# Optimization experiments

Hardware: AMD Instinct MI355X
Metric: run time of the kernel (lower is better)

Reference implementation:

```python
import jax, jax.numpy as jnp
import numpy as np

B, S, D = 2, 4096, 1024
P_DROP = 0.2


def setup_inputs() -> dict:
    key = jax.random.key(0)
    ks = jax.random.split(key, 8)
    scale = 1.0 / np.sqrt(D)
    return {
        "x": jax.random.normal(ks[0], (B, S, D), jnp.float32),
        "Wq": jax.random.normal(ks[1], (D, D), jnp.float32) * scale,
        "bq": jnp.zeros((D,), jnp.float32),
        "Wk": jax.random.normal(ks[2], (D, D), jnp.float32) * scale,
        "bk": jnp.zeros((D,), jnp.float32),
        "Wv": jax.random.normal(ks[3], (D, D), jnp.float32) * scale,
        "bv": jnp.zeros((D,), jnp.float32),
        "dropout_u": jax.random.uniform(ks[4], (B, S, S), jnp.float32),
    }


def reference(x, Wq, bq, Wk, bk, Wv, bv, dropout_u):
    # torch nn.Linear: y = x @ W.T + b
    Q = jnp.einsum("bsd,ed->bse", x, Wq) + bq
    K = jnp.einsum("bsd,ed->bse", x, Wk) + bk
    V = jnp.einsum("bsd,ed->bse", x, Wv) + bv
    # NOTE: original has no 1/sqrt(d) scaling
    scores = jnp.einsum("bqd,bkd->bqk", Q, K)  # [B,S,S]
    attn = jax.nn.softmax(scores, axis=-1)
    # inverted dropout, p=0.2, deterministic mask from dropout_u
    mask = (dropout_u >= P_DROP).astype(attn.dtype) / (1.0 - P_DROP)
    attn = attn * mask
    return jnp.einsum("bqk,bkd->bqd", attn, V)
```

## Files before the change

kernel.cpp:

```cpp
#include <hip/hip_runtime.h>

typedef float    f32x4 __attribute__((ext_vector_type(4)));
typedef _Float16 f16x8 __attribute__((ext_vector_type(8)));
typedef _Float16 f16x4 __attribute__((ext_vector_type(4)));
typedef _Float16 f16;

#define DEVFN static __device__ __forceinline__

constexpr int BB = 2, SS = 4096, DD = 1024;
constexpr int MROWS = BB * SS;

constexpr size_t SZ_QK   = (size_t)MROWS * DD * 2;
constexpr size_t SZ_VT   = (size_t)BB * DD * SS * 2;
constexpr size_t SZ_ATTN = (size_t)BB * SS * SS * 2;
constexpr size_t SZ_S    = (size_t)BB * SS * SS * 4;
constexpr size_t SZ_W    = (size_t)DD * DD * 2;

constexpr size_t O_VT   = 0;
constexpr size_t O_ATTN = O_VT + SZ_VT;
constexpr size_t O_Q    = O_ATTN;
constexpr size_t O_K    = O_Q + 2 * SZ_QK;
constexpr size_t O_S    = O_ATTN + SZ_ATTN;
constexpr size_t O_XH   = O_S;
constexpr size_t O_WQH  = O_XH + SZ_QK;
constexpr size_t O_WKH  = O_WQH + SZ_W;
constexpr size_t O_WVH  = O_WKH + SZ_W;
constexpr size_t WS_NEEDED = SZ_VT + SZ_ATTN + SZ_S;

DEVFN f32x4 mfma16x16x32(f16x8 a, f16x8 b, f32x4 c) {
  return __builtin_amdgcn_mfma_f32_16x16x32_f16(a, b, c, 0, 0, 0);
}

DEVFN void gld16(const f16* g, char* l) {
  __builtin_amdgcn_global_load_lds((const __attribute__((address_space(1))) void*)g,
                                   (__attribute__((address_space(3))) void*)l, 16, 0, 0);
}

DEVFN void swz_xy(int& bx, int& by, int& bz) {
  const int gx = gridDim.x, gy = gridDim.y, gz = gridDim.z;
  const int lin = (blockIdx.z * gy + blockIdx.y) * gx + blockIdx.x;
  const int chunk = (gx * gy * gz) >> 3;
  const int nl = (lin & 7) * chunk + (lin >> 3);
  bx = nl % gx; const int r = nl / gx; by = r % gy; bz = r / gy;
}

DEVFN void gemm128_core(const f16* Ap, const f16* Bp, size_t ld, int NT,
                        char* smem, f32x4 (&acc)[4][4]) {
  const int tid = threadIdx.x, lane = tid & 63, wave = tid >> 6;
  const int wm = wave >> 1, wn = wave & 1;
  const size_t rk = (size_t)(tid >> 3) * ld +
                    (size_t)((((lane & 7) ^ (lane >> 3)) << 3));
  const int wvoff = wave << 10;
  const int rbA = (((wm << 6) + (lane & 15)) << 7);
  const int rbB = (((wn << 6) + (lane & 15)) << 7);
  const int cx0 = (((lane >> 4) << 4)) ^ ((lane & 7) << 4);
  const int cx1 = cx0 ^ 64;

  char* LA0 = smem;
  char* LA1 = smem + 32768;
  char* LA2 = smem + 65536;
  char* LB0 = smem + 98304;
  char* LB1 = smem + 114688;

  auto stA = [&](int u, int q, char* dst) {
    int uc = (u < NT) ? u : (NT - 1);
    gld16(Ap + (size_t)(q << 6) * ld + ((size_t)uc << 6) + rk, dst + (q << 13) + wvoff);
  };
  auto stB = [&](int u, int q, char* dst) {
    int uc = (u < NT) ? u : (NT - 1);
    gld16(Bp + (size_t)(q << 6) * ld + ((size_t)uc << 6) + rk, dst + (q << 13) + wvoff);
  };
  auto rdA = [&](char* l, int m, int cx) { return *(const f16x8*)(l + rbA + (m << 11) + cx); };
  auto rdB = [&](char* l, int n, int cx) { return *(const f16x8*)(l + rbB + (n << 11) + cx); };

  f16x8 A0[2][2], B0[2][2], A0n[2][2], B0n[2][2];

  stA(0, 0, LA0); stA(0, 1, LA0); stA(0, 2, LA0); stA(0, 3, LA0);
  stB(0, 0, LB0); stB(0, 1, LB0);
  stA(1, 0, LA1); stA(1, 1, LA1); stA(1, 2, LA1); stA(1, 3, LA1);
  stB(1, 0, LB1); stB(1, 1, LB1);
  asm volatile("s_waitcnt vmcnt(6)" ::: "memory");
  __builtin_amdgcn_s_barrier();
#pragma unroll
  for (int n = 0; n < 2; ++n) { B0[n][0] = rdB(LB0, n, cx0); B0[n][1] = rdB(LB0, n, cx1); }
#pragma unroll
  for (int m = 0; m < 2; ++m) { A0[m][0] = rdA(LA0, m, cx0); A0[m][1] = rdA(LA0, m, cx1); }

  char *aC = LA0, *aN = LA1, *aN2 = LA2, *bC = LB0, *bN = LB1;

  auto tileX = [&](char* lA, char* lB, char* lAn, char* lA2, char* lBn, int t,
                   f16x8 (&a0)[2][2], f16x8 (&b0)[2][2],
                   f16x8 (&a0n)[2][2], f16x8 (&b0n)[2][2]) {
    f16x8 a1[2][2], b1[2][2];
#pragma unroll
    for (int n = 0; n < 2; ++n) { b1[n][0] = rdB(lB, n + 2, cx0); b1[n][1] = rdB(lB, n + 2, cx1); }
    stA(t + 2, 0, lA2); stA(t + 2, 1, lA2);
    __builtin_amdgcn_s_barrier();
    asm volatile("s_waitcnt lgkmcnt(4)" ::: "memory");
    __builtin_amdgcn_sched_barrier(0);
    __builtin_amdgcn_s_setprio(1);
#pragma unroll
    for (int m = 0; m < 2; ++m)
#pragma unroll
      for (int n = 0; n < 2; ++n) {
        acc[m][n] = mfma16x16x32(a0[m][0], b0[n][0], acc[m][n]);
        acc[m][n] = mfma16x16x32(a0[m][1], b0[n][1], acc[m][n]);
      }
    __builtin_amdgcn_s_setprio(0);
    __builtin_amdgcn_s_barrier();
#pragma unroll
    for (int m = 0; m < 2; ++m) { a1[m][0] = rdA(lA, m + 2, cx0); a1[m][1] = rdA(lA, m + 2, cx1); }
    stA(t + 2, 2, lA2); stA(t + 2, 3, lA2);
    asm volatile("s_waitcnt vmcnt(4)" ::: "memory");
    __builtin_amdgcn_s_barrier();
    asm volatile("s_waitcnt lgkmcnt(4)" ::: "memory");
    __builtin_amdgcn_sched_barrier(0);
    __builtin_amdgcn_s_setprio(1);
#pragma unroll
    for (int m = 0; m < 2; ++m)
#pragma unroll
      for (int n = 0; n < 2; ++n) {
        acc[m][n + 2] = mfma16x16x32(a0[m][0], b1[n][0], acc[m][n + 2]);
        acc[m][n + 2] = mfma16x16x32(a0[m][1], b1[n][1], acc[m][n + 2]);
      }
    __builtin_amdgcn_s_setprio(0);
    __builtin_amdgcn_s_barrier();
#pragma unroll
    for (int n = 0; n < 2; ++n) { b0n[n][0] = rdB(lBn, n, cx0); b0n[n][1] = rdB(lBn, n, cx1); }
    stB(t + 2, 0, lB); stB(t + 2, 1, lB);
    __builtin_amdgcn_s_barrier();
    asm volatile("s_waitcnt lgkmcnt(4)" ::: "memory");
    __builtin_amdgcn_sched_barrier(0);
    __builtin_amdgcn_s_setprio(1);
#pragma unroll
    for (int m = 0; m < 2; ++m)
#pragma unroll
      for (int n = 0; n < 2; ++n) {
        acc[m + 2][n] = mfma16x16x32(a1[m][0], b0[n][0], acc[m + 2][n]);
        acc[m + 2][n] = mfma16x16x32(a1[m][1], b0[n][1], acc[m + 2][n]);
      }
    __builtin_amdgcn_s_setprio(0);
    __builtin_amdgcn_s_barrier();
#pragma unroll
    for (int m = 0; m < 2; ++m) { a0n[m][0] = rdA(lAn, m, cx0); a0n[m][1] = rdA(lAn, m, cx1); }
    __builtin_amdgcn_s_barrier();
    asm volatile("s_waitcnt lgkmcnt(4)" ::: "memory");
    __builtin_amdgcn_sched_barrier(0);
    __builtin_amdgcn_s_setprio(1);
#pragma unroll
    for (int m = 0; m < 2; ++m)
#pragma unroll
      for (int n = 0; n < 2; ++n) {
        acc[m + 2][n + 2] = mfma16x16x32(a1[m][0], b1[n][0], acc[m + 2][n + 2]);
        acc[m + 2][n + 2] = mfma16x16x32(a1[m][1], b1[n][1], acc[m + 2][n + 2]);
      }
    __builtin_amdgcn_s_setprio(0);
    __builtin_amdgcn_s_barrier();
  };

  for (int t = 0; t < NT; t += 2) {
    tileX(aC, bC, aN, aN2, bN, t, A0, B0, A0n, B0n);
    { char* tmp = aC; aC = aN; aN = aN2; aN2 = tmp; }
    { char* tmp = bC; bC = bN; bN = tmp; }
    tileX(aC, bC, aN, aN2, bN, t + 1, A0n, B0n, A0, B0);
    { char* tmp = aC; aC = aN; aN = aN2; aN2 = tmp; }
    { char* tmp = bC; bC = bN; bN = tmp; }
  }
  asm volatile("s_waitcnt vmcnt(0)" ::: "memory");
}

__global__ __launch_bounds__(512, 2)
void gemm_sc128(const f16* __restrict__ Q, const f16* __restrict__ Kp,
                float* __restrict__ Sf) {
  extern __shared__ char smem[];
  int bx, by, bz; swz_xy(bx, by, bz);
  const size_t zo = (size_t)bz * SS * DD;
  const int row0 = by * 256, col0 = bx * 128;
  f32x4 acc[4][4] = {};
  gemm128_core(Q + zo + (size_t)row0 * DD, Kp + zo + (size_t)col0 * DD,
               DD, 16, smem, acc);

  float* C = Sf + (size_t)bz * SS * SS;
  const int lane = threadIdx.x & 63, wave = threadIdx.x >> 6;
  const int wm = wave >> 1, wn = wave & 1;
#pragma unroll
  for (int m = 0; m < 4; ++m)
#pragma unroll
    for (int n = 0; n < 4; ++n) {
      int col = col0 + wn * 64 + n * 16 + (lane & 15);
      int rowb = row0 + wm * 64 + m * 16 + (lane >> 4) * 4;
#pragma unroll
      for (int j = 0; j < 4; ++j)
        __builtin_nontemporal_store(acc[m][n][j], &C[(size_t)(rowb + j) * SS + col]);
    }
}

__global__ __launch_bounds__(512, 2)
void gemm_projqk128(const f16* __restrict__ xh,
                    const f16* __restrict__ wqh, const f16* __restrict__ wkh,
                    const float* __restrict__ bq, const float* __restrict__ bk,
                    f16* __restrict__ Q, f16* __restrict__ K) {
  extern __shared__ char smem[];
  int bx, by, bz; swz_xy(bx, by, bz);
  const int row0 = by * 256;
  const bool isK = bx >= 8;
  const int col0 = (bx & 7) * 128;
  const f16* B0p = isK ? wkh : wqh;
  const float* bias = isK ? bk : bq;
  f16* CH = isK ? K : Q;

  f32x4 acc[4][4] = {};
  gemm128_core(xh + (size_t)row0 * DD, B0p + (size_t)col0 * DD, DD, 16, smem, acc);

  const int lane = threadIdx.x & 63, wave = threadIdx.x >> 6;
  const int wm = wave >> 1, wn = wave & 1;
#pragma unroll
  for (int m = 0; m < 4; ++m)
#pragma unroll
    for (int n = 0; n < 4; ++n) {
      int col = col0 + wn * 64 + n * 16 + (lane & 15);
      float bvv = bias[col];
      int rowb = row0 + wm * 64 + m * 16 + (lane >> 4) * 4;
#pragma unroll
      for (int j = 0; j < 4; ++j)
        CH[(size_t)(rowb + j) * DD + col] = (f16)(acc[m][n][j] + bvv);
    }
}

__global__ __launch_bounds__(512, 2)
void gemm_vt128(const f16* __restrict__ wvh, const f16* __restrict__ xh,
                const float* __restrict__ bvv, f16* __restrict__ Vt) {
  extern __shared__ char smem[];
  int bx, by, bz; swz_xy(bx, by, bz);
  const int row0 = by * 256;
  const int col0 = bx * 128;
  f32x4 acc[4][4] = {};
  gemm128_core(wvh + (size_t)row0 * DD, xh + (size_t)col0 * DD, DD, 16, smem, acc);

  const int lane = threadIdx.x & 63, wave = threadIdx.x >> 6;
  const int wm = wave >> 1, wn = wave & 1;
#pragma unroll
  for (int m = 0; m < 4; ++m)
#pragma unroll
    for (int n = 0; n < 4; ++n) {
      int col = col0 + wn * 64 + n * 16 + (lane & 15);
      int batch = col >> 12, sl = col & 4095;
      int rowb = row0 + wm * 64 + m * 16 + (lane >> 4) * 4;
#pragma unroll
      for (int j = 0; j < 4; ++j) {
        float v = acc[m][n][j] + bvv[rowb + j];
        Vt[(size_t)batch * DD * SS + (size_t)(rowb + j) * SS + sl] = (f16)v;
      }
    }
}

__global__ __launch_bounds__(512, 2)
void gemm_pv128(const f16* __restrict__ Pb, const f16* __restrict__ Vt,
                float* __restrict__ out) {
  extern __shared__ char smem[];
  int bx, by, bz; swz_xy(bx, by, bz);
  const int row0 = by * 256;
  const int col0 = bx * 128;
  f32x4 acc[4][4] = {};
  gemm128_core(Pb + (size_t)bz * SS * SS + (size_t)row0 * SS,
               Vt + (size_t)bz * DD * SS + (size_t)col0 * SS,
               SS, 64, smem, acc);

  float* C = out + (size_t)bz * SS * DD;
  const int lane = threadIdx.x & 63, wave = threadIdx.x >> 6;
  const int wm = wave >> 1, wn = wave & 1;
#pragma unroll
  for (int m = 0; m < 4; ++m)
#pragma unroll
    for (int n = 0; n < 4; ++n) {
      int col = col0 + wn * 64 + n * 16 + (lane & 15);
      int rowb = row0 + wm * 64 + m * 16 + (lane >> 4) * 4;
#pragma unroll
      for (int j = 0; j < 4; ++j)
        __builtin_nontemporal_store(acc[m][n][j], &C[(size_t)(rowb + j) * DD + col]);
    }
}

__global__ __launch_bounds__(256)
void split_all(const float* __restrict__ x, const float* __restrict__ Wq,
               const float* __restrict__ Wk, const float* __restrict__ Wv,
               f16* __restrict__ xh, f16* __restrict__ wqh,
               f16* __restrict__ wkh, f16* __restrict__ wvh) {
  const int b = blockIdx.x, tid = threadIdx.x;
  const float* in; f16* hi; int nv, rb, nb;
  if (b < 1536)      { in = x;  hi = xh;  nv = (MROWS * DD) >> 2; rb = b;        nb = 1536; }
  else if (b < 1792) { in = Wq; hi = wqh; nv = (DD * DD) >> 2;    rb = b - 1536; nb = 256; }
  else if (b < 2048) { in = Wk; hi = wkh; nv = (DD * DD) >> 2;    rb = b - 1792; nb = 256; }
  else               { in = Wv; hi = wvh; nv = (DD * DD) >> 2;    rb = b - 2048; nb = 256; }
  for (int i = rb * 256 + tid; i < nv; i += nb * 256) {
    f32x4 v = *(const f32x4*)(in + (size_t)i * 4);
    f16x4 h;
#pragma unroll
    for (int e = 0; e < 4; ++e) h[e] = (f16)v[e];
    *(f16x4*)(hi + (size_t)i * 4) = h;
  }
}

__global__ __launch_bounds__(256)
void softmax_dropout(const float* __restrict__ Sf, const float* __restrict__ U,
                     f16* __restrict__ P) {
  __shared__ float red[4];
  const size_t row = blockIdx.x;
  const float* s = Sf + row * SS;
  const float* u = U + row * SS;
  f16* p = P + row * SS;
  const int tid = threadIdx.x, lane = tid & 63, wave = tid >> 6;

  f32x4 v[4];
  float m = -3.0e38f;
#pragma unroll
  for (int j = 0; j < 4; ++j) {
    v[j] = __builtin_nontemporal_load((const f32x4*)(s + (size_t)(j * 256 + tid) * 4));
#pragma unroll
    for (int e = 0; e < 4; ++e) m = fmaxf(m, v[j][e]);
  }
#pragma unroll
  for (int o = 32; o > 0; o >>= 1) m = fmaxf(m, __shfl_xor(m, o));
  if (lane == 0) red[wave] = m;
  __syncthreads();
  m = fmaxf(fmaxf(red[0], red[1]), fmaxf(red[2], red[3]));

  float sum = 0.0f;
#pragma unroll
  for (int j = 0; j < 4; ++j)
#pragma unroll
    for (int e = 0; e < 4; ++e) { float ex = __expf(v[j][e] - m); v[j][e] = ex; sum += ex; }
#pragma unroll
  for (int o = 32; o > 0; o >>= 1) sum += __shfl_xor(sum, o);
  __syncthreads();
  if (lane == 0) red[wave] = sum;
  __syncthreads();
  sum = red[0] + red[1] + red[2] + red[3];
  const float scale = 1.25f / sum;

#pragma unroll
  for (int j = 0; j < 4; ++j) {
    f32x4 uu = __builtin_nontemporal_load((const f32x4*)(u + (size_t)(j * 256 + tid) * 4));
    f16x4 out;
#pragma unroll
    for (int e = 0; e < 4; ++e)
      out[e] = (f16)((uu[e] >= 0.2f) ? v[j][e] * scale : 0.0f);
    *(f16x4*)(p + (size_t)(j * 256 + tid) * 4) = out;
  }
}

extern "C" void kernel_launch(void* const* d_in, const int* in_sizes, int n_in,
                              void* d_out, int out_size, void* d_ws, size_t ws_size,
                              hipStream_t stream) {
  if (ws_size < WS_NEEDED) return;

  const float* x  = (const float*)d_in[0];
  const float* Wq = (const float*)d_in[1];
  const float* bq = (const float*)d_in[2];
  const float* Wk = (const float*)d_in[3];
  const float* bk = (const float*)d_in[4];
  const float* Wv = (const float*)d_in[5];
  const float* bv = (const float*)d_in[6];
  const float* du = (const float*)d_in[7];

  char* ws = (char*)d_ws;
  f16*   Vt  = (f16*)(ws + O_VT);
  f16*   Pb  = (f16*)(ws + O_ATTN);
  f16*   Q   = (f16*)(ws + O_Q);
  f16*   K   = (f16*)(ws + O_K);
  float* Sf  = (float*)(ws + O_S);
  f16*   xh  = (f16*)(ws + O_XH);
  f16*   wqh = (f16*)(ws + O_WQH);
  f16*   wkh = (f16*)(ws + O_WKH);
  f16*   wvh = (f16*)(ws + O_WVH);
  float* out = (float*)d_out;

  hipFuncSetAttribute((const void*)gemm_sc128,
                      hipFuncAttributeMaxDynamicSharedMemorySize, 131072);
  hipFuncSetAttribute((const void*)gemm_projqk128,
                      hipFuncAttributeMaxDynamicSharedMemorySize, 131072);
  hipFuncSetAttribute((const void*)gemm_vt128,
                      hipFuncAttributeMaxDynamicSharedMemorySize, 131072);
  hipFuncSetAttribute((const void*)gemm_pv128,
                      hipFuncAttributeMaxDynamicSharedMemorySize, 131072);

  split_all<<<2304, 256, 0, stream>>>(x, Wq, Wk, Wv, xh, wqh, wkh, wvh);

  gemm_projqk128<<<dim3(16, MROWS / 256), 512, 131072, stream>>>(
      xh, wqh, wkh, bq, bk, Q, K);

  gemm_vt128<<<dim3(MROWS / 128, DD / 256), 512, 131072, stream>>>(wvh, xh, bv, Vt);

  gemm_sc128<<<dim3(SS / 128, SS / 256, BB), 512, 131072, stream>>>(Q, K, Sf);

  softmax_dropout<<<MROWS, 256, 0, stream>>>(Sf, du, Pb);

  gemm_pv128<<<dim3(DD / 128, SS / 256, BB), 512, 131072, stream>>>(Pb, Vt, out);
}
```

Baseline: 276.0 us.

## Merge QK and V projection GEMMs into one launch and remap score-GEMM blocks

Merges the Q/K projection kernel and the V-transpose projection kernel into a single 768-block launch, with block ids interleaved across groups of 8. It also replaces the score GEMM's block swizzle with a custom mapping that groups 128 tiles per XCD-style region, and drops the nontemporal stores for the fp32 score matrix. The aim is to cut one launch and tail, balance work across the chip, and keep score tiles cache-resident for the softmax that follows. Removing the nontemporal hint may push useful data out of cache.

```diff
diff --git a/kernel.cpp b/kernel.cpp
--- a/kernel.cpp
+++ b/kernel.cpp
@@ -173,7 +173,13 @@
 void gemm_sc128(const f16* __restrict__ Q, const f16* __restrict__ Kp,
                 float* __restrict__ Sf) {
   extern __shared__ char smem[];
-  int bx, by, bz; swz_xy(bx, by, bz);
+  const int lin = (blockIdx.z * 16 + blockIdx.y) * 32 + blockIdx.x;
+  const int g = (lin & 7) * 128 + (lin >> 3);
+  const int bz = g >> 9;
+  const int w = g & 511;
+  const int t = w >> 7, s = w & 127;
+  const int bx = (t & 1) * 16 + (s & 15);
+  const int by = (t >> 1) * 8 + (s >> 4);
   const size_t zo = (size_t)bz * SS * DD;
   const int row0 = by * 256, col0 = bx * 128;
   f32x4 acc[4][4] = {};
@@ -191,67 +197,64 @@
       int rowb = row0 + wm * 64 + m * 16 + (lane >> 4) * 4;
 #pragma unroll
       for (int j = 0; j < 4; ++j)
-        __builtin_nontemporal_store(acc[m][n][j], &C[(size_t)(rowb + j) * SS + col]);
+        C[(size_t)(rowb + j) * SS + col] = acc[m][n][j];
     }
 }
 
 __global__ __launch_bounds__(512, 2)
-void gemm_projqk128(const f16* __restrict__ xh,
+void gemm_projvt128(const f16* __restrict__ xh,
                     const f16* __restrict__ wqh, const f16* __restrict__ wkh,
+                    const f16* __restrict__ wvh,
                     const float* __restrict__ bq, const float* __restrict__ bk,
-                    f16* __restrict__ Q, f16* __restrict__ K) {
+                    const float* __restrict__ bvv,
+                    f16* __restrict__ Q, f16* __restrict__ K,
+                    f16* __restrict__ Vt) {
   extern __shared__ char smem[];
-  int bx, by, bz; swz_xy(bx, by, bz);
-  const int row0 = by * 256;
-  const bool isK = bx >= 8;
-  const int col0 = (bx & 7) * 128;
-  const f16* B0p = isK ? wkh : wqh;
-  const float* bias = isK ? bk : bq;
-  f16* CH = isK ? K : Q;
-
-  f32x4 acc[4][4] = {};
-  gemm128_core(xh + (size_t)row0 * DD, B0p + (size_t)col0 * DD, DD, 16, smem, acc);
-
+  const int lin = blockIdx.x;
+  const int id = (lin & 7) * 96 + (lin >> 3);
   const int lane = threadIdx.x & 63, wave = threadIdx.x >> 6;
   const int wm = wave >> 1, wn = wave & 1;
-#pragma unroll
-  for (int m = 0; m < 4; ++m)
-#pragma unroll
-    for (int n = 0; n < 4; ++n) {
-      int col = col0 + wn * 64 + n * 16 + (lane & 15);
-      float bvv = bias[col];
-      int rowb = row0 + wm * 64 + m * 16 + (lane >> 4) * 4;
-#pragma unroll
-      for (int j = 0; j < 4; ++j)
-        CH[(size_t)(rowb + j) * DD + col] = (f16)(acc[m][n][j] + bvv);
-    }
-}
-
-__global__ __launch_bounds__(512, 2)
-void gemm_vt128(const f16* __restrict__ wvh, const f16* __restrict__ xh,
-                const float* __restrict__ bvv, f16* __restrict__ Vt) {
-  extern __shared__ char smem[];
-  int bx, by, bz; swz_xy(bx, by, bz);
-  const int row0 = by * 256;
-  const int col0 = bx * 128;
   f32x4 acc[4][4] = {};
-  gemm128_core(wvh + (size_t)row0 * DD, xh + (size_t)col0 * DD, DD, 16, smem, acc);
-
-  const int lane = threadIdx.x & 63, wave = threadIdx.x >> 6;
-  const int wm = wave >> 1, wn = wave & 1;
-#pragma unroll
-  for (int m = 0; m < 4; ++m)
-#pragma unroll
-    for (int n = 0; n < 4; ++n) {
-      int col = col0 + wn * 64 + n * 16 + (lane & 15);
-      int batch = col >> 12, sl = col & 4095;
-      int rowb = row0 + wm * 64 + m * 16 + (lane >> 4) * 4;
-#pragma unroll
-      for (int j = 0; j < 4; ++j) {
-        float v = acc[m][n][j] + bvv[rowb + j];
-        Vt[(size_t)batch * DD * SS + (size_t)(rowb + j) * SS + sl] = (f16)v;
-      }
-    }
+
+  if (id < 512) {
+    const int bx = id & 15, by = id >> 4;
+    const int row0 = by * 256;
+    const bool isK = bx >= 8;
+    const int col0 = (bx & 7) * 128;
+    const f16* B0p = isK ? wkh : wqh;
+    const float* bias = isK ? bk : bq;
+    f16* CH = isK ? K : Q;
+    gemm128_core(xh + (size_t)row0 * DD, B0p + (size_t)col0 * DD, DD, 16, smem, acc);
+#pragma unroll
+    for (int m = 0; m < 4; ++m)
+#pragma unroll
+      for (int n = 0; n < 4; ++n) {
+        int col = col0 + wn * 64 + n * 16 + (lane & 15);
+        float bvv2 = bias[col];
+        int rowb = row0 + wm * 64 + m * 16 + (lane >> 4) * 4;
+#pragma unroll
+        for (int j = 0; j < 4; ++j)
+          CH[(size_t)(rowb + j) * DD + col] = (f16)(acc[m][n][j] + bvv2);
+      }
+  } else {
+    const int id2 = id - 512;
+    const int bx = id2 & 63, by = id2 >> 6;
+    const int row0 = by * 256, col0 = bx * 128;
+    gemm128_core(wvh + (size_t)row0 * DD, xh + (size_t)col0 * DD, DD, 16, smem, acc);
+#pragma unroll
+    for (int m = 0; m < 4; ++m)
+#pragma unroll
+      for (int n = 0; n < 4; ++n) {
+        int col = col0 + wn * 64 + n * 16 + (lane & 15);
+        int batch = col >> 12, sl = col & 4095;
+        int rowb = row0 + wm * 64 + m * 16 + (lane >> 4) * 4;
+#pragma unroll
+        for (int j = 0; j < 4; ++j) {
+          float v = acc[m][n][j] + bvv[rowb + j];
+          Vt[(size_t)batch * DD * SS + (size_t)(rowb + j) * SS + sl] = (f16)v;
+        }
+      }
+  }
 }
 
 __global__ __launch_bounds__(512, 2)
@@ -377,21 +380,17 @@
 
   hipFuncSetAttribute((const void*)gemm_sc128,
                       hipFuncAttributeMaxDynamicSharedMemorySize, 131072);
-  hipFuncSetAttribute((const void*)gemm_projqk128,
-                      hipFuncAttributeMaxDynamicSharedMemorySize, 131072);
-  hipFuncSetAttribute((const void*)gemm_vt128,
+  hipFuncSetAttribute((const void*)gemm_projvt128,
                       hipFuncAttributeMaxDynamicSharedMemorySize, 131072);
   hipFuncSetAttribute((const void*)gemm_pv128,
                       hipFuncAttributeMaxDynamicSharedMemorySize, 131072);
 
   split_all<<<2304, 256, 0, stream>>>(x, Wq, Wk, Wv, xh, wqh, wkh, wvh);
 
-  gemm_projqk128<<<dim3(16, MROWS / 256), 512, 131072, stream>>>(
-      xh, wqh, wkh, bq, bk, Q, K);
-
-  gemm_vt128<<<dim3(MROWS / 128, DD / 256), 512, 131072, stream>>>(wvh, xh, bv, Vt);
-
-  gemm_sc128<<<dim3(SS / 128, SS / 256, BB), 512, 131072, stream>>>(Q, K, Sf);
+  gemm_projvt128<<<768, 512, 131072, stream>>>(
+      xh, wqh, wkh, wvh, bq, bk, bv, Q, K, Vt);
+
+  gemm_sc128<<<dim3(32, 16, BB), 512, 131072, stream>>>(Q, K, Sf);
 
   softmax_dropout<<<MROWS, 256, 0, stream>>>(Sf, du, Pb);
 
```

New measurement: 258.8 us, median of 2. 6.2% less time.
